# Optimization experiments

Hardware: AMD Instinct MI355X
Metric: run time of the kernel (lower is better)

## Reference

```python
import jax, jax.numpy as jnp
import numpy as np

D_MODEL = 256
N_HEADS = 8
N_LEVELS = 3
N_POINTS = 4
D_HEAD = D_MODEL // N_HEADS
SHAPES = [(128, 128), (64, 64), (32, 32)]  # (H, W) per level
BS = 8
NQ = 900


def setup_inputs() -> dict:
    key = jax.random.key(0)
    ks = jax.random.split(key, 13)
    sum_hw = sum(h * w for h, w in SHAPES)
    s = 0.02
    starts = np.cumsum([0] + [h * w for h, w in SHAPES[:-1]]).astype(np.int32)
    return {
        "query": jax.random.normal(ks[0], (BS, NQ, D_MODEL), jnp.float32),
        "reference_points": jax.random.uniform(ks[1], (BS, NQ, N_LEVELS, 2), jnp.float32),
        "input_flatten": jax.random.normal(ks[2], (BS, sum_hw, D_MODEL), jnp.float32),
        "spatial_shapes": jnp.array(SHAPES, jnp.int32),
        "level_start_index": jnp.array(starts, jnp.int32),
        "W_off": jax.random.normal(ks[3], (D_MODEL, N_HEADS * N_LEVELS * N_POINTS * 2), jnp.float32) * s,
        "b_off": jax.random.normal(ks[4], (N_HEADS * N_LEVELS * N_POINTS * 2,), jnp.float32),
        "W_attn": jax.random.normal(ks[5], (D_MODEL, N_HEADS * N_LEVELS * N_POINTS), jnp.float32) * s,
        "b_attn": jax.random.normal(ks[6], (N_HEADS * N_LEVELS * N_POINTS,), jnp.float32) * s,
        "W_val": jax.random.normal(ks[7], (D_MODEL, D_MODEL), jnp.float32) * s,
        "b_val": jnp.zeros((D_MODEL,), jnp.float32),
        "W_out": jax.random.normal(ks[8], (D_MODEL, D_MODEL), jnp.float32) * s,
        "b_out": jnp.zeros((D_MODEL,), jnp.float32),
    }


def _msda(query, reference_points, input_flatten, shapes_np, starts_np,
          W_off, b_off, W_attn, b_attn, W_val, b_val, W_out, b_out):
    bs, nq, _ = query.shape
    # value projection -> [bs, sum_hw, H, Dh]
    value = (input_flatten @ W_val + b_val).reshape(bs, -1, N_HEADS, D_HEAD)
    # learned offsets and attention weights
    offsets = (query @ W_off + b_off).reshape(bs, nq, N_HEADS, N_LEVELS, N_POINTS, 2)
    attn = (query @ W_attn + b_attn).reshape(bs, nq, N_HEADS, N_LEVELS * N_POINTS)
    attn = jax.nn.softmax(attn, axis=-1).reshape(bs, nq, N_HEADS, N_LEVELS, N_POINTS)

    bidx = jnp.arange(bs)[:, None, None, None]
    hidx = jnp.arange(N_HEADS)[None, None, :, None]
    acc = jnp.zeros((bs, nq, N_HEADS, D_HEAD), value.dtype)
    for l in range(N_LEVELS):
        Hl, Wl = int(shapes_np[l, 0]), int(shapes_np[l, 1])
        st = int(starts_np[l])
        # [bs, H, Hl*Wl, Dh]
        v = jnp.transpose(value[:, st:st + Hl * Wl], (0, 2, 1, 3))
        norm = jnp.array([Wl, Hl], value.dtype)
        # sampling locations in [0,1] -> pixel coords (grid_sample align_corners=False)
        loc = reference_points[:, :, None, l, None, :] + offsets[:, :, :, l] / norm
        px = loc[..., 0] * Wl - 0.5  # [bs, nq, H, P]
        py = loc[..., 1] * Hl - 0.5
        x0 = jnp.floor(px); y0 = jnp.floor(py)
        lx = px - x0; ly = py - y0
        x0i = x0.astype(jnp.int32); y0i = y0.astype(jnp.int32)

        def gather(ix, iy):
            valid = (ix >= 0) & (ix < Wl) & (iy >= 0) & (iy < Hl)
            flat = jnp.clip(iy, 0, Hl - 1) * Wl + jnp.clip(ix, 0, Wl - 1)
            g = v[bidx, hidx, flat]  # [bs, nq, H, P, Dh]
            return g * valid[..., None].astype(v.dtype)

        samp = (gather(x0i, y0i) * ((1 - lx) * (1 - ly))[..., None]
                + gather(x0i + 1, y0i) * (lx * (1 - ly))[..., None]
                + gather(x0i, y0i + 1) * ((1 - lx) * ly)[..., None]
                + gather(x0i + 1, y0i + 1) * (lx * ly)[..., None])
        acc = acc + jnp.einsum('bqhp,bqhpd->bqhd', attn[:, :, :, l], samp)

    return acc.reshape(bs, nq, D_MODEL) @ W_out + b_out


def reference(query, reference_points, input_flatten, spatial_shapes, level_start_index,
              W_off, b_off, W_attn, b_attn, W_val, b_val, W_out, b_out):
    shapes_np = np.asarray(spatial_shapes)
    starts_np = np.asarray(level_start_index)
    return _msda(query, reference_points, input_flatten, shapes_np, starts_np,
                 W_off, b_off, W_attn, b_attn, W_val, b_val, W_out, b_out)
```

## Files before the change

### kernel.cpp

```cpp
#include <hip/hip_runtime.h>
#include <hip/hip_bf16.h>

typedef __bf16 bf16;
typedef bf16 bf16x8 __attribute__((ext_vector_type(8)));
typedef float f32x4 __attribute__((ext_vector_type(4)));

#define BSZ 8
#define NQ 900
#define NH 8
#define SUMHW 21504
#define NROW 7200

#define BIGF 3.3e38f

__device__ inline float ld_rt(const void* p, size_t i, int f32) {
  return f32 ? ((const float*)p)[i] : (float)((const bf16*)p)[i];
}

__device__ inline void stage16_rt(const void* p, size_t i, bf16* dst, int f32) {
  if (f32) {
    const float* s = (const float*)p + i;
    bf16x8 lo, hi;
#pragma unroll
    for (int j = 0; j < 2; ++j) {
      float4 v0 = ((const float4*)s)[2 * j];
      float4 v1 = ((const float4*)s)[2 * j + 1];
      bf16x8& d = j ? hi : lo;
      d[0] = (bf16)v0.x; d[1] = (bf16)v0.y; d[2] = (bf16)v0.z; d[3] = (bf16)v0.w;
      d[4] = (bf16)v1.x; d[5] = (bf16)v1.y; d[6] = (bf16)v1.z; d[7] = (bf16)v1.w;
    }
    *(bf16x8*)dst = lo;
    *(bf16x8*)(dst + 8) = hi;
  } else {
    const bf16* s = (const bf16*)p + i;
    *(bf16x8*)dst = *(const bf16x8*)s;
    *(bf16x8*)(dst + 8) = *(const bf16x8*)(s + 8);
  }
}

__global__ void probe_flags(const bf16* q, int* flags) {
  if (threadIdx.x != 0 || blockIdx.x != 0) return;
  int c = 0;
  for (int i = 0; i < 512; ++i) {
    float x = (float)q[i];
    if (!(fabsf(x) <= 1000.f)) c++;
  }
  flags[0] = (c > 32) ? 1 : 0;
  flags[1] = 0;
  flags[2] = 0;
}

__global__ __launch_bounds__(256) void transpose256(const void* __restrict__ in,
                                                    bf16* __restrict__ out,
                                                    const int* __restrict__ flags) {
  const int f32 = flags[0];
  int idx = blockIdx.x * 256 + threadIdx.x;
  int k = idx >> 8, n = idx & 255;
  out[n * 256 + k] = (bf16)ld_rt(in, idx, f32);
}

__global__ __launch_bounds__(256) void transpose_oa(const void* __restrict__ Woff,
                                                    const void* __restrict__ Wattn,
                                                    bf16* __restrict__ Wt,
                                                    const int* __restrict__ flags) {
  const int f32 = flags[0];
  int idx = blockIdx.x * 256 + threadIdx.x;
  int n = idx >> 8, k = idx & 255;
  float v = (n < 192) ? ld_rt(Woff, (size_t)k * 192 + n, f32)
                      : ld_rt(Wattn, (size_t)k * 96 + (n - 192), f32);
  Wt[idx] = (bf16)v;
}

template <typename TC>
__global__ __launch_bounds__(256) void gemm_nt_256(
    const void* __restrict__ A, const bf16* __restrict__ Wt,
    const void* __restrict__ bias, TC* __restrict__ C, int rowbase, int M,
    const int* __restrict__ aflags, const int* __restrict__ bflags) {
  __shared__ __align__(16) bf16 As[64][72];
  __shared__ __align__(16) bf16 Bs[256][72];
  const int af32 = aflags[0], bf32 = bflags[0];
  const int t = threadIdx.x;
  const int w = t >> 6, lane = t & 63;
  const int ml = lane & 15, qd = lane >> 4;
  const int blockM = blockIdx.x * 64;
  f32x4 acc[16] = {};

  for (int k0 = 0; k0 < 256; k0 += 64) {
    int r = t >> 2, c = (t & 3) * 16;
    int row = blockM + r;
    if (row > M - 1) row = M - 1;
    stage16_rt(A, ((size_t)rowbase + row) * 256 + k0 + c, &As[r][c], af32);
    const bf16* wsrc = Wt + t * 256 + k0;
#pragma unroll
    for (int j = 0; j < 8; ++j)
      *(bf16x8*)&Bs[t][j * 8] = *(const bf16x8*)(wsrc + j * 8);
    __syncthreads();
#pragma unroll
    for (int kc = 0; kc < 2; ++kc) {
      bf16x8 a = *(const bf16x8*)&As[w * 16 + ml][kc * 32 + qd * 8];
#pragma unroll
      for (int tn = 0; tn < 16; ++tn) {
        bf16x8 bb = *(const bf16x8*)&Bs[tn * 16 + ml][kc * 32 + qd * 8];
        acc[tn] = __builtin_amdgcn_mfma_f32_16x16x32_bf16(a, bb, acc[tn], 0, 0, 0);
      }
    }
    __syncthreads();
  }

#pragma unroll
  for (int tn = 0; tn < 16; ++tn) {
    int col = tn * 16 + ml;
    float bv = ld_rt(bias, col, bf32);
#pragma unroll
    for (int rr = 0; rr < 4; ++rr) {
      int row = blockM + w * 16 + qd * 4 + rr;
      float v = fminf(fmaxf(acc[tn][rr] + bv, -BIGF), BIGF);
      if (row < M) C[((size_t)rowbase + row) * 256 + col] = (TC)v;
    }
  }
}

__global__ __launch_bounds__(256) void gemm_oa(const void* __restrict__ query,
                                               const bf16* __restrict__ Wt,
                                               const void* __restrict__ boff,
                                               const void* __restrict__ battn,
                                               float* __restrict__ offs,
                                               float* __restrict__ logits,
                                               const int* __restrict__ flags) {
  __shared__ __align__(16) bf16 As[64][72];
  __shared__ __align__(16) bf16 Bs[288][72];
  const int f32 = flags[0];
  const int t = threadIdx.x;
  const int w = t >> 6, lane = t & 63;
  const int ml = lane & 15, qd = lane >> 4;
  const int blockM = blockIdx.x * 64;
  f32x4 acc[18] = {};

  for (int k0 = 0; k0 < 256; k0 += 64) {
    int r = t >> 2, c = (t & 3) * 16;
    int row = blockM + r;
    if (row > NROW - 1) row = NROW - 1;
    stage16_rt(query, (size_t)row * 256 + k0 + c, &As[r][c], f32);
    const bf16* wsrc = Wt + t * 256 + k0;
#pragma unroll
    for (int j = 0; j < 8; ++j)
      *(bf16x8*)&Bs[t][j * 8] = *(const bf16x8*)(wsrc + j * 8);
    if (t < 32) {
      const bf16* wsrc2 = Wt + (256 + t) * 256 + k0;
#pragma unroll
      for (int j = 0; j < 8; ++j)
        *(bf16x8*)&Bs[256 + t][j * 8] = *(const bf16x8*)(wsrc2 + j * 8);
    }
    __syncthreads();
#pragma unroll
    for (int kc = 0; kc < 2; ++kc) {
      bf16x8 a = *(const bf16x8*)&As[w * 16 + ml][kc * 32 + qd * 8];
#pragma unroll
      for (int tn = 0; tn < 18; ++tn) {
        bf16x8 bb = *(const bf16x8*)&Bs[tn * 16 + ml][kc * 32 + qd * 8];
        acc[tn] = __builtin_amdgcn_mfma_f32_16x16x32_bf16(a, bb, acc[tn], 0, 0, 0);
      }
    }
    __syncthreads();
  }

#pragma unroll
  for (int tn = 0; tn < 18; ++tn) {
    int col = tn * 16 + ml;
#pragma unroll
    for (int rr = 0; rr < 4; ++rr) {
      int row = blockM + w * 16 + qd * 4 + rr;
      if (row < NROW) {
        float v = acc[tn][rr];
        if (col < 192)
          offs[(size_t)row * 192 + col] = v + ld_rt(boff, col, f32);
        else
          logits[(size_t)row * 96 + (col - 192)] = v + ld_rt(battn, col - 192, f32);
      }
    }
  }
}

__global__ __launch_bounds__(256) void msda_sample(
    const bf16* __restrict__ value, const void* __restrict__ refp,
    const float* __restrict__ offs, const float* __restrict__ logits,
    bf16* __restrict__ accb, int b_base, size_t batch_stride,
    const int* __restrict__ flags) {
  const int f32 = flags[0];
  const int qi = blockIdx.x, bl = blockIdx.y;
  const int b = b_base + bl;
  const int row = b * NQ + qi;
  const int t = threadIdx.x, h = t >> 5, d = t & 31;
  const bf16* valb = value + (size_t)bl * batch_stride;

  const float* lg = logits + (size_t)(row * NH + h) * 12;
  float lv[12];
#pragma unroll
  for (int i = 0; i < 12; ++i) lv[i] = fminf(fmaxf(lg[i], -BIGF), BIGF);
  float mx = -BIGF;
#pragma unroll
  for (int i = 0; i < 12; ++i) mx = fmaxf(mx, lv[i]);
  float e[12], se = 0.f;
#pragma unroll
  for (int i = 0; i < 12; ++i) {
    e[i] = __expf(lv[i] - mx);
    se += e[i];
  }
  const float inv = 1.f / se;

  const float* of = offs + (size_t)(row * NH + h) * 24;
  const int Hs[3] = {128, 64, 32}, Wd[3] = {128, 64, 32}, st[3] = {0, 16384, 20480};
  float acc = 0.f;
#pragma unroll
  for (int l = 0; l < 3; ++l) {
    const int Hl = Hs[l], Wl = Wd[l];
    float rx = ld_rt(refp, (size_t)(row * 3 + l) * 2 + 0, f32);
    float ry = ld_rt(refp, (size_t)(row * 3 + l) * 2 + 1, f32);
    const bf16* base = valb + (size_t)st[l] * 256 + h * 32 + d;
#pragma unroll
    for (int p = 0; p < 4; ++p) {
      float ox = of[(l * 4 + p) * 2 + 0], oy = of[(l * 4 + p) * 2 + 1];
      float px = (rx + ox / (float)Wl) * (float)Wl - 0.5f;
      float py = (ry + oy / (float)Hl) * (float)Hl - 0.5f;
      px = fminf(fmaxf(px, -1e6f), 1e6f);
      py = fminf(fmaxf(py, -1e6f), 1e6f);
      const float x0f = floorf(px), y0f = floorf(py);
      const float lx = px - x0f, ly = py - y0f;
      const int x0 = (int)x0f, y0 = (int)y0f;
      const float wgt = e[l * 4 + p] * inv;
      float s = 0.f;
#pragma unroll
      for (int cy = 0; cy < 2; ++cy) {
        const int iy = y0 + cy;
        const float wy = cy ? ly : 1.f - ly;
        const bool vy = (iy >= 0) && (iy < Hl);
        const int iyc = iy < 0 ? 0 : (iy > Hl - 1 ? Hl - 1 : iy);
#pragma unroll
        for (int cx = 0; cx < 2; ++cx) {
          const int ix = x0 + cx;
          const float wx = cx ? lx : 1.f - lx;
          const bool vx = (ix >= 0) && (ix < Wl);
          const int ixc = ix < 0 ? 0 : (ix > Wl - 1 ? Wl - 1 : ix);
          float g = (float)base[(size_t)(iyc * Wl + ixc) * 256];
          g = fminf(fmaxf(g, -BIGF), BIGF);
          s += (vx && vy) ? wx * wy * g : 0.f;
        }
      }
      acc += wgt * s;
    }
  }
  accb[(size_t)row * 256 + t] = (bf16)acc;
}

extern "C" void kernel_launch(void* const* d_in, const int* in_sizes, int n_in,
                              void* d_out, int out_size, void* d_ws, size_t ws_size,
                              hipStream_t stream) {
  const void* query = d_in[0];
  const void* refp = d_in[1];
  const void* inpf = d_in[2];
  const void* W_off = d_in[5];
  const void* b_off = d_in[6];
  const void* W_attn = d_in[7];
  const void* b_attn = d_in[8];
  const void* W_val = d_in[9];
  const void* b_val = d_in[10];
  const void* W_out = d_in[11];
  const void* b_out = d_in[12];

  float* out = (float*)d_out;
  char* ws = (char*)d_ws;
  int* flags = (int*)ws;
  const int* bf16flag = flags + 2;
  bf16* Wt_val = (bf16*)(ws + 256);
  bf16* Wt_out = (bf16*)(ws + 131328);
  bf16* Wt_oa = (bf16*)(ws + 262400);
  float* offs = (float*)(ws + 409856);
  float* logits = (float*)(ws + 5939456);
  bf16* accb = (bf16*)(ws + 8704256);
  bf16* value = (bf16*)(ws + 12390656);
  const unsigned long long WS_FULL = 12390656ULL + 88080384ULL;
  const unsigned long long WS_TIGHT = 12390656ULL + 11010048ULL;

  const int pipeline_ok = ws_size >= WS_TIGHT;
  const int full = ws_size >= WS_FULL;

  probe_flags<<<1, 64, 0, stream>>>((const bf16*)query, flags);
  if (pipeline_ok) {
    transpose256<<<256, 256, 0, stream>>>(W_val, Wt_val, flags);
    transpose256<<<256, 256, 0, stream>>>(W_out, Wt_out, flags);
    transpose_oa<<<288, 256, 0, stream>>>(W_off, W_attn, Wt_oa, flags);
    gemm_oa<<<(NROW + 63) / 64, 256, 0, stream>>>(query, Wt_oa, b_off, b_attn, offs,
                                                  logits, flags);
    if (full) {
      gemm_nt_256<bf16><<<(BSZ * SUMHW) / 64, 256, 0, stream>>>(
          inpf, Wt_val, b_val, value, 0, BSZ * SUMHW, flags, flags);
      msda_sample<<<dim3(NQ, BSZ), 256, 0, stream>>>(
          value, refp, offs, logits, accb, 0, (size_t)SUMHW * 256, flags);
    } else {
      for (int b = 0; b < BSZ; ++b) {
        gemm_nt_256<bf16><<<SUMHW / 64, 256, 0, stream>>>(
            inpf, Wt_val, b_val, value - (size_t)b * SUMHW * 256, b * SUMHW, SUMHW,
            flags, flags);
        msda_sample<<<dim3(NQ, 1), 256, 0, stream>>>(value, refp, offs, logits, accb,
                                                     b, 0, flags);
      }
    }
    gemm_nt_256<float><<<(NROW + 63) / 64, 256, 0, stream>>>(
        accb, Wt_out, b_out, out, 0, NROW, bf16flag, flags);
  }
}
```

Baseline: 463.4 us.

## Replace LDS-staged GEMMs with single-wave direct-load MFMA kernels

```diff
diff --git a/kernel.cpp b/kernel.cpp
--- a/kernel.cpp
+++ b/kernel.cpp
@@ -17,37 +17,32 @@
   return f32 ? ((const float*)p)[i] : (float)((const bf16*)p)[i];
 }
 
-__device__ inline void stage16_rt(const void* p, size_t i, bf16* dst, int f32) {
+__device__ inline bf16x8 load_a8(const void* p, size_t i, int f32) {
   if (f32) {
-    const float* s = (const float*)p + i;
-    bf16x8 lo, hi;
-#pragma unroll
-    for (int j = 0; j < 2; ++j) {
-      float4 v0 = ((const float4*)s)[2 * j];
-      float4 v1 = ((const float4*)s)[2 * j + 1];
-      bf16x8& d = j ? hi : lo;
-      d[0] = (bf16)v0.x; d[1] = (bf16)v0.y; d[2] = (bf16)v0.z; d[3] = (bf16)v0.w;
-      d[4] = (bf16)v1.x; d[5] = (bf16)v1.y; d[6] = (bf16)v1.z; d[7] = (bf16)v1.w;
-    }
-    *(bf16x8*)dst = lo;
-    *(bf16x8*)(dst + 8) = hi;
-  } else {
-    const bf16* s = (const bf16*)p + i;
-    *(bf16x8*)dst = *(const bf16x8*)s;
-    *(bf16x8*)(dst + 8) = *(const bf16x8*)(s + 8);
-  }
+    const float4* s = (const float4*)((const float*)p + i);
+    float4 v0 = s[0], v1 = s[1];
+    bf16x8 d;
+    d[0] = (bf16)v0.x; d[1] = (bf16)v0.y; d[2] = (bf16)v0.z; d[3] = (bf16)v0.w;
+    d[4] = (bf16)v1.x; d[5] = (bf16)v1.y; d[6] = (bf16)v1.z; d[7] = (bf16)v1.w;
+    return d;
+  }
+  return *(const bf16x8*)((const bf16*)p + i);
 }
 
 __global__ void probe_flags(const bf16* q, int* flags) {
-  if (threadIdx.x != 0 || blockIdx.x != 0) return;
+  const int lane = threadIdx.x;
   int c = 0;
-  for (int i = 0; i < 512; ++i) {
+  for (int i = lane; i < 512; i += 64) {
     float x = (float)q[i];
     if (!(fabsf(x) <= 1000.f)) c++;
   }
-  flags[0] = (c > 32) ? 1 : 0;
-  flags[1] = 0;
-  flags[2] = 0;
+#pragma unroll
+  for (int m = 1; m < 64; m <<= 1) c += __shfl_xor(c, m, 64);
+  if (lane == 0) {
+    flags[0] = (c > 32) ? 1 : 0;
+    flags[1] = 0;
+    flags[2] = 0;
+  }
 }
 
 __global__ __launch_bounds__(256) void transpose256(const void* __restrict__ in,
@@ -72,113 +67,87 @@
 }
 
 template <typename TC>
-__global__ __launch_bounds__(256) void gemm_nt_256(
+__global__ __launch_bounds__(64) void gemm_stream(
     const void* __restrict__ A, const bf16* __restrict__ Wt,
     const void* __restrict__ bias, TC* __restrict__ C, int rowbase, int M,
     const int* __restrict__ aflags, const int* __restrict__ bflags) {
-  __shared__ __align__(16) bf16 As[64][72];
-  __shared__ __align__(16) bf16 Bs[256][72];
   const int af32 = aflags[0], bf32 = bflags[0];
-  const int t = threadIdx.x;
-  const int w = t >> 6, lane = t & 63;
+  const int lane = threadIdx.x;
   const int ml = lane & 15, qd = lane >> 4;
-  const int blockM = blockIdx.x * 64;
-  f32x4 acc[16] = {};
-
-  for (int k0 = 0; k0 < 256; k0 += 64) {
-    int r = t >> 2, c = (t & 3) * 16;
-    int row = blockM + r;
-    if (row > M - 1) row = M - 1;
-    stage16_rt(A, ((size_t)rowbase + row) * 256 + k0 + c, &As[r][c], af32);
-    const bf16* wsrc = Wt + t * 256 + k0;
-#pragma unroll
-    for (int j = 0; j < 8; ++j)
-      *(bf16x8*)&Bs[t][j * 8] = *(const bf16x8*)(wsrc + j * 8);
-    __syncthreads();
-#pragma unroll
-    for (int kc = 0; kc < 2; ++kc) {
-      bf16x8 a = *(const bf16x8*)&As[w * 16 + ml][kc * 32 + qd * 8];
-#pragma unroll
-      for (int tn = 0; tn < 16; ++tn) {
-        bf16x8 bb = *(const bf16x8*)&Bs[tn * 16 + ml][kc * 32 + qd * 8];
-        acc[tn] = __builtin_amdgcn_mfma_f32_16x16x32_bf16(a, bb, acc[tn], 0, 0, 0);
-      }
-    }
-    __syncthreads();
-  }
-
-#pragma unroll
-  for (int tn = 0; tn < 16; ++tn) {
-    int col = tn * 16 + ml;
-    float bv = ld_rt(bias, col, bf32);
-#pragma unroll
-    for (int rr = 0; rr < 4; ++rr) {
-      int row = blockM + w * 16 + qd * 4 + rr;
-      float v = fminf(fmaxf(acc[tn][rr] + bv, -BIGF), BIGF);
-      if (row < M) C[((size_t)rowbase + row) * 256 + col] = (TC)v;
-    }
-  }
-}
-
-__global__ __launch_bounds__(256) void gemm_oa(const void* __restrict__ query,
-                                               const bf16* __restrict__ Wt,
-                                               const void* __restrict__ boff,
-                                               const void* __restrict__ battn,
-                                               float* __restrict__ offs,
-                                               float* __restrict__ logits,
-                                               const int* __restrict__ flags) {
-  __shared__ __align__(16) bf16 As[64][72];
-  __shared__ __align__(16) bf16 Bs[288][72];
-  const int f32 = flags[0];
-  const int t = threadIdx.x;
-  const int w = t >> 6, lane = t & 63;
+  const int blockM = blockIdx.x * 32;
+  f32x4 acc[2][16] = {};
+
+  const size_t ar0 = ((size_t)rowbase + blockM + ml) * 256;
+  const size_t ar1 = ar0 + 16 * 256;
+
+  for (int ks = 0; ks < 8; ++ks) {
+    const int kof = ks * 32 + qd * 8;
+    bf16x8 a0 = load_a8(A, ar0 + kof, af32);
+    bf16x8 a1 = load_a8(A, ar1 + kof, af32);
+#pragma unroll
+    for (int tn = 0; tn < 16; ++tn) {
+      bf16x8 bb = *(const bf16x8*)(Wt + (size_t)(tn * 16 + ml) * 256 + kof);
+      acc[0][tn] = __builtin_amdgcn_mfma_f32_16x16x32_bf16(a0, bb, acc[0][tn], 0, 0, 0);
+      acc[1][tn] = __builtin_amdgcn_mfma_f32_16x16x32_bf16(a1, bb, acc[1][tn], 0, 0, 0);
+    }
+  }
+
+#pragma unroll
+  for (int m = 0; m < 2; ++m)
+#pragma unroll
+    for (int tn = 0; tn < 16; ++tn) {
+      int col = tn * 16 + ml;
+      float bv = ld_rt(bias, col, bf32);
+#pragma unroll
+      for (int rr = 0; rr < 4; ++rr) {
+        int row = blockM + m * 16 + qd * 4 + rr;
+        float v = fminf(fmaxf(acc[m][tn][rr] + bv, -BIGF), BIGF);
+        C[((size_t)rowbase + row) * 256 + col] = (TC)v;
+      }
+    }
+}
+
+__global__ __launch_bounds__(64) void gemm_oa_stream(
+    const void* __restrict__ query, const bf16* __restrict__ Wt,
+    const void* __restrict__ boff, const void* __restrict__ battn,
+    float* __restrict__ offs, float* __restrict__ logits,
+    const int* __restrict__ flags) {
+  const int f32 = flags[0];
+  const int lane = threadIdx.x;
   const int ml = lane & 15, qd = lane >> 4;
-  const int blockM = blockIdx.x * 64;
-  f32x4 acc[18] = {};
-
-  for (int k0 = 0; k0 < 256; k0 += 64) {
-    int r = t >> 2, c = (t & 3) * 16;
-    int row = blockM + r;
-    if (row > NROW - 1) row = NROW - 1;
-    stage16_rt(query, (size_t)row * 256 + k0 + c, &As[r][c], f32);
-    const bf16* wsrc = Wt + t * 256 + k0;
-#pragma unroll
-    for (int j = 0; j < 8; ++j)
-      *(bf16x8*)&Bs[t][j * 8] = *(const bf16x8*)(wsrc + j * 8);
-    if (t < 32) {
-      const bf16* wsrc2 = Wt + (256 + t) * 256 + k0;
-#pragma unroll
-      for (int j = 0; j < 8; ++j)
-        *(bf16x8*)&Bs[256 + t][j * 8] = *(const bf16x8*)(wsrc2 + j * 8);
-    }
-    __syncthreads();
-#pragma unroll
-    for (int kc = 0; kc < 2; ++kc) {
-      bf16x8 a = *(const bf16x8*)&As[w * 16 + ml][kc * 32 + qd * 8];
-#pragma unroll
-      for (int tn = 0; tn < 18; ++tn) {
-        bf16x8 bb = *(const bf16x8*)&Bs[tn * 16 + ml][kc * 32 + qd * 8];
-        acc[tn] = __builtin_amdgcn_mfma_f32_16x16x32_bf16(a, bb, acc[tn], 0, 0, 0);
-      }
-    }
-    __syncthreads();
-  }
-
-#pragma unroll
-  for (int tn = 0; tn < 18; ++tn) {
-    int col = tn * 16 + ml;
-#pragma unroll
-    for (int rr = 0; rr < 4; ++rr) {
-      int row = blockM + w * 16 + qd * 4 + rr;
-      if (row < NROW) {
-        float v = acc[tn][rr];
+  const int blockM = blockIdx.x * 32;
+  f32x4 acc[2][18] = {};
+
+  const size_t ar0 = ((size_t)blockM + ml) * 256;
+  const size_t ar1 = ar0 + 16 * 256;
+
+  for (int ks = 0; ks < 8; ++ks) {
+    const int kof = ks * 32 + qd * 8;
+    bf16x8 a0 = load_a8(query, ar0 + kof, f32);
+    bf16x8 a1 = load_a8(query, ar1 + kof, f32);
+#pragma unroll
+    for (int tn = 0; tn < 18; ++tn) {
+      bf16x8 bb = *(const bf16x8*)(Wt + (size_t)(tn * 16 + ml) * 256 + kof);
+      acc[0][tn] = __builtin_amdgcn_mfma_f32_16x16x32_bf16(a0, bb, acc[0][tn], 0, 0, 0);
+      acc[1][tn] = __builtin_amdgcn_mfma_f32_16x16x32_bf16(a1, bb, acc[1][tn], 0, 0, 0);
+    }
+  }
+
+#pragma unroll
+  for (int m = 0; m < 2; ++m)
+#pragma unroll
+    for (int tn = 0; tn < 18; ++tn) {
+      int col = tn * 16 + ml;
+#pragma unroll
+      for (int rr = 0; rr < 4; ++rr) {
+        int row = blockM + m * 16 + qd * 4 + rr;
+        float v = acc[m][tn][rr];
         if (col < 192)
           offs[(size_t)row * 192 + col] = v + ld_rt(boff, col, f32);
         else
           logits[(size_t)row * 96 + (col - 192)] = v + ld_rt(battn, col - 192, f32);
       }
     }
-  }
 }
 
 __global__ __launch_bounds__(256) void msda_sample(
@@ -289,23 +258,23 @@
     transpose256<<<256, 256, 0, stream>>>(W_val, Wt_val, flags);
     transpose256<<<256, 256, 0, stream>>>(W_out, Wt_out, flags);
     transpose_oa<<<288, 256, 0, stream>>>(W_off, W_attn, Wt_oa, flags);
-    gemm_oa<<<(NROW + 63) / 64, 256, 0, stream>>>(query, Wt_oa, b_off, b_attn, offs,
-                                                  logits, flags);
+    gemm_oa_stream<<<NROW / 32, 64, 0, stream>>>(query, Wt_oa, b_off, b_attn, offs,
+                                                 logits, flags);
     if (full) {
-      gemm_nt_256<bf16><<<(BSZ * SUMHW) / 64, 256, 0, stream>>>(
+      gemm_stream<bf16><<<(BSZ * SUMHW) / 32, 64, 0, stream>>>(
           inpf, Wt_val, b_val, value, 0, BSZ * SUMHW, flags, flags);
       msda_sample<<<dim3(NQ, BSZ), 256, 0, stream>>>(
           value, refp, offs, logits, accb, 0, (size_t)SUMHW * 256, flags);
     } else {
       for (int b = 0; b < BSZ; ++b) {
-        gemm_nt_256<bf16><<<SUMHW / 64, 256, 0, stream>>>(
+        gemm_stream<bf16><<<SUMHW / 32, 64, 0, stream>>>(
             inpf, Wt_val, b_val, value - (size_t)b * SUMHW * 256, b * SUMHW, SUMHW,
             flags, flags);
         msda_sample<<<dim3(NQ, 1), 256, 0, stream>>>(value, refp, offs, logits, accb,
                                                      b, 0, flags);
       }
     }
-    gemm_nt_256<float><<<(NROW + 63) / 64, 256, 0, stream>>>(
+    gemm_stream<float><<<NROW / 32, 64, 0, stream>>>(
         accb, Wt_out, b_out, out, 0, NROW, bf16flag, flags);
   }
 }
```

Result: slower. 629.4 us (+35.8%).
